# Performance work log

Hardware: AMD Instinct MI355X
Metric: run time of the kernel (lower is better)

## Reference

```python
import jax, jax.numpy as jnp
import numpy as np

N, E, M = 8192, 32768, 2048
D, H1, C = 768, 8, 768
NEG_SLOPE = 0.2


def gat_conv(x, src, dst, W, att_src, att_dst, bias, heads, out_ch):
    # PyG GATConv (eval mode, concat=True, add_self_loops already applied to src/dst)
    n = x.shape[0]
    h = (x @ W).reshape(n, heads, out_ch)                      # [N,H,C]
    a_src = jnp.einsum('nhc,hc->nh', h, att_src)               # [N,H]
    a_dst = jnp.einsum('nhc,hc->nh', h, att_dst)
    e = jax.nn.leaky_relu(a_src[src] + a_dst[dst], NEG_SLOPE)  # [E',H]
    # softmax over incoming edges of each dst node
    m = jax.ops.segment_max(e, dst, num_segments=n)
    e = jnp.exp(e - m[dst])
    denom = jax.ops.segment_sum(e, dst, num_segments=n)
    alpha = e / (denom[dst] + 1e-16)                           # [E',H]
    msg = h[src] * alpha[:, :, None]                           # [E',H,C]
    out = jax.ops.segment_sum(msg, dst, num_segments=n)        # [N,H,C]
    return out.reshape(n, heads * out_ch) + bias


def setup_inputs() -> dict:
    key = jax.random.key(0)
    ks = jax.random.split(key, 16)
    s = 0.02
    inp = {
        'x': jax.random.normal(ks[0], (N, D), jnp.float32),
        'edge_index': jax.random.randint(ks[1], (2, E), 0, N, jnp.int64),
        'mask_idx': jax.random.randint(ks[2], (M,), 0, N, jnp.int64),
        'W1': jax.random.normal(ks[3], (D, H1 * C), jnp.float32) * s,
        'att_src1': jax.random.normal(ks[4], (H1, C), jnp.float32) * s,
        'att_dst1': jax.random.normal(ks[5], (H1, C), jnp.float32) * s,
        'b1': jnp.zeros((H1 * C,), jnp.float32),
        'W2': jax.random.normal(ks[6], (H1 * C, C), jnp.float32) * s,
        'att_src2': jax.random.normal(ks[7], (1, C), jnp.float32) * s,
        'att_dst2': jax.random.normal(ks[8], (1, C), jnp.float32) * s,
        'b2': jnp.zeros((C,), jnp.float32),
        # fc: 1536 -> 768, classifier: 768 -> 2
        'fc_w': jax.random.normal(ks[9], (2 * C, C), jnp.float32) * s,
        'fc_b': jnp.zeros((C,), jnp.float32),
        'cls_w': jax.random.normal(ks[10], (C, 2), jnp.float32) * s,
        'cls_b': jnp.zeros((2,), jnp.float32),
    }
    return inp


def reference(x, edge_index, mask_idx, W1, att_src1, att_dst1, b1,
              W2, att_src2, att_dst2, b2, fc_w, fc_b, cls_w, cls_b):
    n = x.shape[0]
    loops = jnp.arange(n, dtype=edge_index.dtype)
    src = jnp.concatenate([edge_index[0], loops])   # PyG default add_self_loops
    dst = jnp.concatenate([edge_index[1], loops])
    h = gat_conv(x, src, dst, W1, att_src1, att_dst1, b1, H1, C)   # [N, 6144]
    h = jax.nn.elu(h)
    h = gat_conv(h, src, dst, W2, att_src2, att_dst2, b2, 1, C)    # [N, 768]
    x_gemb = h[mask_idx]                                           # [M, 768]
    x_emb = x[mask_idx]                                            # [M, 768]
    out = jnp.concatenate([x_gemb, x_emb], axis=1) @ fc_w + fc_b   # [M, 768]
    out = out @ cls_w + cls_b                                      # [M, 2]
    return out
```

## Files before the change

### kernel.cpp

```cpp
#include <hip/hip_runtime.h>

typedef unsigned short ushort_t;
typedef __attribute__((ext_vector_type(8))) __bf16 bf16x8;
typedef __attribute__((ext_vector_type(8))) unsigned short ushort8;
typedef __attribute__((ext_vector_type(4))) unsigned short ushort4v;
typedef __attribute__((ext_vector_type(4))) float f32x4;

#define N_NODES 8192
#define NODE_MASK 8191
#define E_EDGES 32768
#define E_TOT   40960
#define M_MASK  2048
#define D_IN    768
#define C_CH    768
#define F1      6144

typedef __attribute__((address_space(1))) const void* gas_ptr;
typedef __attribute__((address_space(3))) void* las_ptr;

__device__ __forceinline__ float bf2f(ushort_t u) {
    union { unsigned int i; float f; } v; v.i = ((unsigned int)u) << 16; return v.f;
}
__device__ __forceinline__ ushort_t f2bf(float f) {
    union { float f; unsigned int i; } v; v.f = f;
    unsigned int r = v.i + 0x7fffu + ((v.i >> 16) & 1u);
    return (ushort_t)(r >> 16);
}

__global__ void init_kernel(int* deg, int* fill, int* flags) {
    int i = blockIdx.x * 256 + threadIdx.x;
    if (i < N_NODES) { deg[i] = 0; fill[i] = 0; }
    if (i < 2) flags[i] = 0;
}
__global__ void detect_kernel(const int* __restrict__ raw, int nhalf, int* __restrict__ flag) {
    int i = blockIdx.x * 256 + threadIdx.x;
    if (i < nhalf && raw[2 * i + 1] != 0) atomicOr(flag, 1);
}
__global__ void convert_idx_kernel(const void* __restrict__ raw, int n,
                                   const int* __restrict__ flag, int* __restrict__ out) {
    int i = blockIdx.x * 256 + threadIdx.x;
    if (i >= n) return;
    int v = (*flag) ? ((const int*)raw)[i] : (int)((const long long*)raw)[i];
    out[i] = v & NODE_MASK;
}

__global__ void cvt_bf16_kernel(const float* __restrict__ in, ushort_t* __restrict__ out, int n4) {
    int i = blockIdx.x * 256 + threadIdx.x;
    if (i >= n4) return;
    f32x4 v = *(const f32x4*)(in + i * 4);
    ushort_t o0 = f2bf(v[0]), o1 = f2bf(v[1]), o2 = f2bf(v[2]), o3 = f2bf(v[3]);
    unsigned long long pk = (unsigned long long)o0 | ((unsigned long long)o1 << 16)
                          | ((unsigned long long)o2 << 32) | ((unsigned long long)o3 << 48);
    *(unsigned long long*)(out + i * 4) = pk;
}

__global__ __launch_bounds__(256) void transpose_cvt_kernel(
    const float* __restrict__ in, ushort_t* __restrict__ out, int R, int Ccols)
{
    __shared__ ushort_t tile[32][33];
    int tx = threadIdx.x & 31, ty = threadIdx.x >> 5;
    int x  = blockIdx.x * 32 + tx;
    int y0 = blockIdx.y * 32;
#pragma unroll
    for (int i = 0; i < 4; ++i)
        tile[ty + i * 8][tx] = f2bf(in[(size_t)(y0 + ty + i * 8) * Ccols + x]);
    __syncthreads();
#pragma unroll
    for (int i = 0; i < 4; ++i)
        out[(size_t)(blockIdx.x * 32 + ty + i * 8) * R + y0 + tx] = tile[tx][ty + i * 8];
}

__global__ __launch_bounds__(256) void gemm_bt_kernel(
    const ushort_t* __restrict__ A, const ushort_t* __restrict__ Bt,
    ushort_t* __restrict__ C, const float* __restrict__ bias,
    int M, int N, int K)
{
    __shared__ ushort_t lsA[128 * 64];
    __shared__ ushort_t lsB[128 * 64];

    const int tid  = threadIdx.x;
    const int lane = tid & 63;
    const int wave = tid >> 6;
    const int wm = wave >> 1, wn = wave & 1;
    const int bx = blockIdx.x, by = blockIdx.y;

    const f32x4 zero = {0.f, 0.f, 0.f, 0.f};
    f32x4 acc[4][4];
#pragma unroll
    for (int i = 0; i < 4; ++i)
#pragma unroll
        for (int j = 0; j < 4; ++j) acc[i][j] = zero;

    const int l8 = lane >> 3;
    const int c8 = lane & 7;
    const int q  = lane >> 4;
    const int rl = lane & 15;

    for (int kt = 0; kt < K; kt += 64) {
        __syncthreads();
#pragma unroll
        for (int i = 0; i < 4; ++i) {
            int rbase = wave * 32 + i * 8;
            int row   = rbase + l8;
            int gch   = c8 ^ (row & 7);
            const ushort_t* gA = A  + (size_t)(by * 128 + row) * K + kt + gch * 8;
            const ushort_t* gB = Bt + (size_t)(bx * 128 + row) * K + kt + gch * 8;
            __builtin_amdgcn_global_load_lds((gas_ptr)gA, (las_ptr)(lsA + rbase * 64), 16, 0, 0);
            __builtin_amdgcn_global_load_lds((gas_ptr)gB, (las_ptr)(lsB + rbase * 64), 16, 0, 0);
        }
        __syncthreads();
#pragma unroll
        for (int s = 0; s < 2; ++s) {
            bf16x8 af[4], bfv[4];
#pragma unroll
            for (int i = 0; i < 4; ++i) {
                int Ra = wm * 64 + i * 16 + rl;
                af[i]  = *(const bf16x8*)(lsA + Ra * 64 + (((s * 4 + q) ^ (Ra & 7)) * 8));
                int Rb = wn * 64 + i * 16 + rl;
                bfv[i] = *(const bf16x8*)(lsB + Rb * 64 + (((s * 4 + q) ^ (Rb & 7)) * 8));
            }
#pragma unroll
            for (int i = 0; i < 4; ++i)
#pragma unroll
                for (int j = 0; j < 4; ++j)
                    acc[i][j] = __builtin_amdgcn_mfma_f32_16x16x32_bf16(af[i], bfv[j], acc[i][j], 0, 0, 0);
        }
    }
#pragma unroll
    for (int j = 0; j < 4; ++j) {
        int col = bx * 128 + wn * 64 + j * 16 + rl;
        float bv = bias ? bias[col] : 0.0f;
#pragma unroll
        for (int i = 0; i < 4; ++i) {
#pragma unroll
            for (int t = 0; t < 4; ++t) {
                int row = by * 128 + wm * 64 + i * 16 + q * 4 + t;
                C[(size_t)row * N + col] = f2bf(acc[i][j][t] + bv);
            }
        }
    }
}

__global__ void indeg_kernel(const int* __restrict__ eic, int* __restrict__ deg) {
    int e = blockIdx.x * 256 + threadIdx.x;
    if (e >= E_TOT) return;
    int dst = (e < E_EDGES) ? eic[E_EDGES + e] : (e - E_EDGES);
    atomicAdd(&deg[dst], 1);
}
__global__ __launch_bounds__(256) void scan_kernel(const int* __restrict__ deg, int* __restrict__ rowptr) {
    __shared__ int part[256];
    int t = threadIdx.x;
    int local[32];
    int s = 0;
#pragma unroll
    for (int i = 0; i < 32; ++i) { local[i] = deg[t * 32 + i]; s += local[i]; }
    part[t] = s;
    __syncthreads();
    for (int off = 1; off < 256; off <<= 1) {
        int v = (t >= off) ? part[t - off] : 0;
        __syncthreads();
        part[t] += v;
        __syncthreads();
    }
    int run = (t == 0) ? 0 : part[t - 1];
#pragma unroll
    for (int i = 0; i < 32; ++i) { rowptr[t * 32 + i] = run; run += local[i]; }
    if (t == 255) rowptr[N_NODES] = run;
}
__global__ void scatter_kernel(const int* __restrict__ eic, const int* __restrict__ rowptr,
                               int* __restrict__ fill, int* __restrict__ csr_src) {
    int e = blockIdx.x * 256 + threadIdx.x;
    if (e >= E_TOT) return;
    int src, dst;
    if (e < E_EDGES) { src = eic[e]; dst = eic[E_EDGES + e]; }
    else             { src = e - E_EDGES; dst = src; }
    int pos = rowptr[dst] + atomicAdd(&fill[dst], 1);
    csr_src[pos] = src;
}

__global__ __launch_bounds__(256) void att_kernel(
    const ushort_t* __restrict__ h, const float* __restrict__ att_s,
    const float* __restrict__ att_d, float* __restrict__ a_s, float* __restrict__ a_d,
    int heads, int stride)
{
    int gid  = blockIdx.x * 4 + (threadIdx.x >> 6);
    int lane = threadIdx.x & 63;
    int n = gid / heads, hd = gid % heads;
    const ushort_t* hp = h + (size_t)n * stride + hd * C_CH;
    const float* sp = att_s + hd * C_CH;
    const float* dp = att_d + hd * C_CH;
    float s1 = 0.f, s2 = 0.f;
#pragma unroll
    for (int j = 0; j < 3; ++j) {
        int o = j * 256 + lane * 4;
        ushort4v hv = *(const ushort4v*)(hp + o);
        f32x4 sv = *(const f32x4*)(sp + o);
        f32x4 dv = *(const f32x4*)(dp + o);
#pragma unroll
        for (int k = 0; k < 4; ++k) {
            float f = bf2f(hv[k]);
            s1 += f * sv[k];
            s2 += f * dv[k];
        }
    }
#pragma unroll
    for (int off = 32; off > 0; off >>= 1) {
        s1 += __shfl_down(s1, off);
        s2 += __shfl_down(s2, off);
    }
    if (lane == 0) { a_s[gid] = s1; a_d[gid] = s2; }
}

__global__ __launch_bounds__(192) void agg8_kernel(
    const ushort_t* __restrict__ h, const float* __restrict__ a_s, const float* __restrict__ a_d,
    const int* __restrict__ rowptr, const int* __restrict__ csr_src,
    const float* __restrict__ bias, ushort_t* __restrict__ out)
{
    const int n = blockIdx.x;
    const int half = blockIdx.y;
    const int tid = threadIdx.x;
    const int base = rowptr[n];
    const int deg  = rowptr[n + 1] - base;

    __shared__ float s_m[8], s_rd[8], s_adst[8];
    __shared__ int   s_src[64];
    __shared__ float s_w[64][8];

    if (tid < 8) {
        float adst = a_d[n * 8 + tid];
        float m = -1e30f;
        for (int e = 0; e < deg; ++e) {
            float scv = a_s[csr_src[base + e] * 8 + tid] + adst;
            scv = scv > 0.f ? scv : 0.2f * scv;
            m = fmaxf(m, scv);
        }
        float den = 0.f;
        for (int e = 0; e < deg; ++e) {
            float scv = a_s[csr_src[base + e] * 8 + tid] + adst;
            scv = scv > 0.f ? scv : 0.2f * scv;
            den += __expf(scv - m);
        }
        s_m[tid] = m; s_rd[tid] = 1.0f / (den + 1e-16f); s_adst[tid] = adst;
    }
    __syncthreads();

    float acc[16];
#pragma unroll
    for (int i = 0; i < 16; ++i) acc[i] = 0.f;
    const int c0   = half * 3072 + tid * 16;
    const int myhd = (half << 2) + tid / 48;

    for (int cs = 0; cs < deg; cs += 64) {
        int cnt = min(64, deg - cs);
        __syncthreads();
        for (int idx = tid; idx < cnt; idx += 192) s_src[idx] = csr_src[base + cs + idx];
        __syncthreads();
        for (int idx = tid; idx < cnt * 8; idx += 192) {
            int e = idx >> 3, hd = idx & 7;
            float scv = a_s[s_src[e] * 8 + hd] + s_adst[hd];
            scv = scv > 0.f ? scv : 0.2f * scv;
            s_w[e][hd] = __expf(scv - s_m[hd]) * s_rd[hd];
        }
        __syncthreads();
        int e = 0;
        for (; e + 1 < cnt; e += 2) {
            const ushort_t* hp0 = h + (size_t)s_src[e] * F1 + c0;
            const ushort_t* hp1 = h + (size_t)s_src[e + 1] * F1 + c0;
            ushort8 a0 = *(const ushort8*)(hp0);
            ushort8 a1 = *(const ushort8*)(hp0 + 8);
            ushort8 b0 = *(const ushort8*)(hp1);
            ushort8 b1 = *(const ushort8*)(hp1 + 8);
            float w0 = s_w[e][myhd], w1 = s_w[e + 1][myhd];
#pragma unroll
            for (int i = 0; i < 8; ++i) {
                acc[i]     += w0 * bf2f(a0[i]) + w1 * bf2f(b0[i]);
                acc[8 + i] += w0 * bf2f(a1[i]) + w1 * bf2f(b1[i]);
            }
        }
        if (e < cnt) {
            const ushort_t* hp0 = h + (size_t)s_src[e] * F1 + c0;
            ushort8 a0 = *(const ushort8*)(hp0);
            ushort8 a1 = *(const ushort8*)(hp0 + 8);
            float w0 = s_w[e][myhd];
#pragma unroll
            for (int i = 0; i < 8; ++i) {
                acc[i]     += w0 * bf2f(a0[i]);
                acc[8 + i] += w0 * bf2f(a1[i]);
            }
        }
    }
#pragma unroll
    for (int i = 0; i < 16; ++i) {
        float v = acc[i] + bias[c0 + i];
        v = v > 0.f ? v : (__expf(v) - 1.0f);
        out[(size_t)n * F1 + c0 + i] = f2bf(v);
    }
}

__global__ __launch_bounds__(256) void agg1_kernel(
    const ushort_t* __restrict__ h, const float* __restrict__ a_s, const float* __restrict__ a_d,
    const int* __restrict__ rowptr, const int* __restrict__ csr_src,
    const float* __restrict__ bias, ushort_t* __restrict__ out)
{
    const int n = blockIdx.x;
    const int tid = threadIdx.x;
    const int base = rowptr[n];
    const int deg  = rowptr[n + 1] - base;
    __shared__ float s_m, s_rd, s_adst;
    __shared__ int   s_src[64];
    __shared__ float s_w[64];
    if (tid == 0) {
        float adst = a_d[n];
        float m = -1e30f;
        for (int e = 0; e < deg; ++e) {
            float scv = a_s[csr_src[base + e]] + adst;
            scv = scv > 0.f ? scv : 0.2f * scv;
            m = fmaxf(m, scv);
        }
        float den = 0.f;
        for (int e = 0; e < deg; ++e) {
            float scv = a_s[csr_src[base + e]] + adst;
            scv = scv > 0.f ? scv : 0.2f * scv;
            den += __expf(scv - m);
        }
        s_m = m; s_rd = 1.0f / (den + 1e-16f); s_adst = adst;
    }
    __syncthreads();
    float acc0 = 0.f, acc1 = 0.f, acc2 = 0.f;
    const int c0 = tid * 3;
    for (int cs = 0; cs < deg; cs += 64) {
        int cnt = min(64, deg - cs);
        __syncthreads();
        for (int idx = tid; idx < cnt; idx += 256) s_src[idx] = csr_src[base + cs + idx];
        __syncthreads();
        for (int idx = tid; idx < cnt; idx += 256) {
            float scv = a_s[s_src[idx]] + s_adst;
            scv = scv > 0.f ? scv : 0.2f * scv;
            s_w[idx] = __expf(scv - s_m) * s_rd;
        }
        __syncthreads();
        for (int e = 0; e < cnt; ++e) {
            const ushort_t* hp = h + (size_t)s_src[e] * C_CH + c0;
            float w = s_w[e];
            acc0 += w * bf2f(hp[0]);
            acc1 += w * bf2f(hp[1]);
            acc2 += w * bf2f(hp[2]);
        }
    }
    out[(size_t)n * C_CH + c0 + 0] = f2bf(acc0 + bias[c0 + 0]);
    out[(size_t)n * C_CH + c0 + 1] = f2bf(acc1 + bias[c0 + 1]);
    out[(size_t)n * C_CH + c0 + 2] = f2bf(acc2 + bias[c0 + 2]);
}

__global__ void gatherfc_kernel(const ushort_t* __restrict__ out2, const ushort_t* __restrict__ xb,
                                const int* __restrict__ maskc, ushort_t* __restrict__ Afc)
{
    int m = blockIdx.x, t = threadIdx.x;
    int mi = maskc[m];
    const ushort_t* p1 = out2 + (size_t)mi * 768;
    const ushort_t* p2 = xb   + (size_t)mi * 768;
    for (int c = t; c < 768; c += 256) {
        Afc[(size_t)m * 1536 + c]       = p1[c];
        Afc[(size_t)m * 1536 + 768 + c] = p2[c];
    }
}

__global__ __launch_bounds__(256) void cls_kernel(
    const ushort_t* __restrict__ fc_out, const float* __restrict__ cls_w,
    const float* __restrict__ cls_b, float* __restrict__ out)
{
    int m = blockIdx.x * 4 + (threadIdx.x >> 6);
    int lane = threadIdx.x & 63;
    float a0 = 0.f, a1 = 0.f;
    const ushort_t* row = fc_out + (size_t)m * 768;
    for (int i = lane; i < 768; i += 64) {
        float v = bf2f(row[i]);
        a0 += v * cls_w[i * 2 + 0];
        a1 += v * cls_w[i * 2 + 1];
    }
#pragma unroll
    for (int off = 32; off > 0; off >>= 1) {
        a0 += __shfl_down(a0, off);
        a1 += __shfl_down(a1, off);
    }
    if (lane == 0) {
        out[m * 2 + 0] = a0 + cls_b[0];
        out[m * 2 + 1] = a1 + cls_b[1];
    }
}

extern "C" void kernel_launch(void* const* d_in, const int* in_sizes, int n_in,
                              void* d_out, int out_size, void* d_ws, size_t ws_size,
                              hipStream_t stream)
{
    const float* x        = (const float*)d_in[0];
    const void*  ei_raw   = d_in[1];
    const void*  mask_raw = d_in[2];
    const float* W1       = (const float*)d_in[3];
    const float* att_src1 = (const float*)d_in[4];
    const float* att_dst1 = (const float*)d_in[5];
    const float* b1       = (const float*)d_in[6];
    const float* W2       = (const float*)d_in[7];
    const float* att_src2 = (const float*)d_in[8];
    const float* att_dst2 = (const float*)d_in[9];
    const float* b2       = (const float*)d_in[10];
    const float* fc_w     = (const float*)d_in[11];
    const float* fc_b     = (const float*)d_in[12];
    const float* cls_w    = (const float*)d_in[13];
    const float* cls_b    = (const float*)d_in[14];
    float* out = (float*)d_out;

    char* ws = (char*)d_ws;
    size_t off = 0;
    auto alloc = [&](size_t bytes) { char* p = ws + off; off = (off + bytes + 255) & ~(size_t)255; return p; };
    int*   flags  = (int*)alloc(2 * 4);
    int*   eic    = (int*)alloc((size_t)2 * E_EDGES * 4);
    int*   maskc  = (int*)alloc((size_t)M_MASK * 4);
    int*   deg    = (int*)alloc(N_NODES * 4);
    int*   fill   = (int*)alloc(N_NODES * 4);
    int*   rowptr = (int*)alloc((N_NODES + 1) * 4);
    int*   csr    = (int*)alloc(E_TOT * 4);
    float* a_s1   = (float*)alloc((size_t)N_NODES * 8 * 4);
    float* a_d1   = (float*)alloc((size_t)N_NODES * 8 * 4);
    float* a_s2   = (float*)alloc((size_t)N_NODES * 4);
    float* a_d2   = (float*)alloc((size_t)N_NODES * 4);
    ushort_t* W1t  = (ushort_t*)alloc((size_t)D_IN * F1 * 2);
    ushort_t* W2t  = (ushort_t*)alloc((size_t)F1 * C_CH * 2);
    ushort_t* fcwt = (ushort_t*)alloc((size_t)1536 * 768 * 2);
    ushort_t* xb   = (ushort_t*)alloc((size_t)N_NODES * D_IN * 2);
    char* region1 = alloc((size_t)N_NODES * F1 * 2);
    char* region2 = alloc((size_t)N_NODES * F1 * 2);
    ushort_t* h1    = (ushort_t*)region1;
    ushort_t* h2    = (ushort_t*)region1;
    ushort_t* Afc   = (ushort_t*)(region1 + (16u << 20));
    ushort_t* fcout = (ushort_t*)(region1 + (32u << 20));
    ushort_t* out1  = (ushort_t*)region2;
    ushort_t* out2  = (ushort_t*)region2;

    init_kernel<<<N_NODES / 256, 256, 0, stream>>>(deg, fill, flags);
    detect_kernel<<<(E_EDGES + 255) / 256, 256, 0, stream>>>((const int*)ei_raw, E_EDGES, &flags[0]);
    detect_kernel<<<(M_MASK / 2 + 255) / 256, 256, 0, stream>>>((const int*)mask_raw, M_MASK / 2, &flags[1]);
    convert_idx_kernel<<<(2 * E_EDGES + 255) / 256, 256, 0, stream>>>(ei_raw, 2 * E_EDGES, &flags[0], eic);
    convert_idx_kernel<<<(M_MASK + 255) / 256, 256, 0, stream>>>(mask_raw, M_MASK, &flags[1], maskc);
    indeg_kernel<<<E_TOT / 256, 256, 0, stream>>>(eic, deg);
    scan_kernel<<<1, 256, 0, stream>>>(deg, rowptr);
    scatter_kernel<<<E_TOT / 256, 256, 0, stream>>>(eic, rowptr, fill, csr);

    cvt_bf16_kernel<<<(N_NODES * D_IN / 4 + 255) / 256, 256, 0, stream>>>(x, xb, N_NODES * D_IN / 4);
    transpose_cvt_kernel<<<dim3(F1 / 32, D_IN / 32), 256, 0, stream>>>(W1, W1t, D_IN, F1);
    transpose_cvt_kernel<<<dim3(C_CH / 32, F1 / 32), 256, 0, stream>>>(W2, W2t, F1, C_CH);
    transpose_cvt_kernel<<<dim3(768 / 32, 1536 / 32), 256, 0, stream>>>(fc_w, fcwt, 1536, 768);

    gemm_bt_kernel<<<dim3(F1 / 128, N_NODES / 128), 256, 0, stream>>>(xb, W1t, h1, nullptr, N_NODES, F1, D_IN);
    att_kernel<<<(N_NODES * 8) / 4, 256, 0, stream>>>(h1, att_src1, att_dst1, a_s1, a_d1, 8, F1);
    agg8_kernel<<<dim3(N_NODES, 2), 192, 0, stream>>>(h1, a_s1, a_d1, rowptr, csr, b1, out1);

    gemm_bt_kernel<<<dim3(C_CH / 128, N_NODES / 128), 256, 0, stream>>>(out1, W2t, h2, nullptr, N_NODES, C_CH, F1);
    att_kernel<<<N_NODES / 4, 256, 0, stream>>>(h2, att_src2, att_dst2, a_s2, a_d2, 1, C_CH);
    agg1_kernel<<<N_NODES, 256, 0, stream>>>(h2, a_s2, a_d2, rowptr, csr, b2, out2);

    gatherfc_kernel<<<M_MASK, 256, 0, stream>>>(out2, xb, maskc, Afc);
    gemm_bt_kernel<<<dim3(768 / 128, M_MASK / 128), 256, 0, stream>>>(Afc, fcwt, fcout, fc_b, M_MASK, 768, 1536);
    cls_kernel<<<M_MASK / 4, 256, 0, stream>>>(fcout, cls_w, cls_b, out);
}
```

Before: 546.1 us.

## Remap GEMM blocks per XCD, unroll aggregation by four, vectorize gather

The GEMM kernel now remaps its linear block index so that consecutive row-blocks are grouped onto the same XCD (block index modulo 8), which is meant to improve L2 reuse of shared A/B tiles. The layer-1 aggregation loop processes four neighbor edges per iteration instead of two, putting more independent gathers in flight at the cost of more registers. The mask gather kernel copies 4-element vectors instead of scalars. Together these target L2 locality, memory-level parallelism and load instruction count.

```diff
diff --git a/kernel.cpp b/kernel.cpp
--- a/kernel.cpp
+++ b/kernel.cpp
@@ -82,7 +82,14 @@
     const int lane = tid & 63;
     const int wave = tid >> 6;
     const int wm = wave >> 1, wn = wave & 1;
-    const int bx = blockIdx.x, by = blockIdx.y;
+
+    const int GX = gridDim.x, GY = gridDim.y;
+    const int lin = blockIdx.y * GX + blockIdx.x;
+    const int byg = (GY >= 8) ? (GY >> 3) : 1;
+    const int xcd = lin & 7;
+    const int jj  = lin >> 3;
+    const int bx  = jj / byg;
+    const int by  = (GY >= 8) ? (xcd * byg + (jj % byg)) : blockIdx.y;
 
     const f32x4 zero = {0.f, 0.f, 0.f, 0.f};
     f32x4 acc[4][4];
@@ -263,24 +270,26 @@
         }
         __syncthreads();
         int e = 0;
-        for (; e + 1 < cnt; e += 2) {
-            const ushort_t* hp0 = h + (size_t)s_src[e] * F1 + c0;
-            const ushort_t* hp1 = h + (size_t)s_src[e + 1] * F1 + c0;
-            ushort8 a0 = *(const ushort8*)(hp0);
-            ushort8 a1 = *(const ushort8*)(hp0 + 8);
-            ushort8 b0 = *(const ushort8*)(hp1);
-            ushort8 b1 = *(const ushort8*)(hp1 + 8);
+        for (; e + 3 < cnt; e += 4) {
+            const ushort_t* p0 = h + (size_t)s_src[e]     * F1 + c0;
+            const ushort_t* p1 = h + (size_t)s_src[e + 1] * F1 + c0;
+            const ushort_t* p2 = h + (size_t)s_src[e + 2] * F1 + c0;
+            const ushort_t* p3 = h + (size_t)s_src[e + 3] * F1 + c0;
+            ushort8 a0 = *(const ushort8*)(p0), a1 = *(const ushort8*)(p0 + 8);
+            ushort8 b0 = *(const ushort8*)(p1), b1 = *(const ushort8*)(p1 + 8);
+            ushort8 c0v = *(const ushort8*)(p2), c1v = *(const ushort8*)(p2 + 8);
+            ushort8 d0 = *(const ushort8*)(p3), d1 = *(const ushort8*)(p3 + 8);
             float w0 = s_w[e][myhd], w1 = s_w[e + 1][myhd];
+            float w2 = s_w[e + 2][myhd], w3 = s_w[e + 3][myhd];
 #pragma unroll
             for (int i = 0; i < 8; ++i) {
-                acc[i]     += w0 * bf2f(a0[i]) + w1 * bf2f(b0[i]);
-                acc[8 + i] += w0 * bf2f(a1[i]) + w1 * bf2f(b1[i]);
+                acc[i]     += w0 * bf2f(a0[i]) + w1 * bf2f(b0[i]) + w2 * bf2f(c0v[i]) + w3 * bf2f(d0[i]);
+                acc[8 + i] += w0 * bf2f(a1[i]) + w1 * bf2f(b1[i]) + w2 * bf2f(c1v[i]) + w3 * bf2f(d1[i]);
             }
         }
-        if (e < cnt) {
-            const ushort_t* hp0 = h + (size_t)s_src[e] * F1 + c0;
-            ushort8 a0 = *(const ushort8*)(hp0);
-            ushort8 a1 = *(const ushort8*)(hp0 + 8);
+        for (; e < cnt; ++e) {
+            const ushort_t* p0 = h + (size_t)s_src[e] * F1 + c0;
+            ushort8 a0 = *(const ushort8*)(p0), a1 = *(const ushort8*)(p0 + 8);
             float w0 = s_w[e][myhd];
 #pragma unroll
             for (int i = 0; i < 8; ++i) {
@@ -357,12 +366,11 @@
 {
     int m = blockIdx.x, t = threadIdx.x;
     int mi = maskc[m];
-    const ushort_t* p1 = out2 + (size_t)mi * 768;
-    const ushort_t* p2 = xb   + (size_t)mi * 768;
-    for (int c = t; c < 768; c += 256) {
-        Afc[(size_t)m * 1536 + c]       = p1[c];
-        Afc[(size_t)m * 1536 + 768 + c] = p2[c];
-    }
+    const ushort4v* p1 = (const ushort4v*)(out2 + (size_t)mi * 768);
+    const ushort4v* p2 = (const ushort4v*)(xb   + (size_t)mi * 768);
+    ushort4v* q1 = (ushort4v*)(Afc + (size_t)m * 1536);
+    ushort4v* q2 = (ushort4v*)(Afc + (size_t)m * 1536 + 768);
+    if (t < 192) { q1[t] = p1[t]; q2[t] = p2[t]; }
 }
 
 __global__ __launch_bounds__(256) void cls_kernel(
```

Measured after the change: 562.2 us. 3.0% more time.
